# Kernel tuning notes

Hardware: AMD Instinct MI355X
Metric: run time of the kernel (lower is better)

The kernel has to match this reference:

```python
import jax, jax.numpy as jnp
import numpy as np

N_ATOMS = 50000
N_PAIRS = 1600000
N_BASIS = 128
N_FILTERS = 128
N_RBF = 20
LOG2 = float(np.log(2.0))


def ssp(x):
    # ShiftedSoftplus: softplus(x) - log(2)
    return jax.nn.softplus(x) - LOG2


def setup_inputs() -> dict:
    key = jax.random.key(0)
    ks = jax.random.split(key, 16)

    def lin(k, fan_in, fan_out):
        bound = 1.0 / np.sqrt(fan_in)
        kw, kb = jax.random.split(k)
        W = jax.random.uniform(kw, (fan_in, fan_out), jnp.float32, -bound, bound)
        b = jax.random.uniform(kb, (fan_out,), jnp.float32, -bound, bound)
        return W, b

    W_in, b_in = lin(ks[0], N_BASIS, N_FILTERS)
    Wf1, bf1 = lin(ks[1], N_RBF, N_FILTERS)
    Wf2, bf2 = lin(ks[2], N_FILTERS, N_FILTERS)
    Wo1, bo1 = lin(ks[3], N_FILTERS, N_BASIS)
    Wo2, bo2 = lin(ks[4], N_BASIS, N_BASIS)

    return {
        "x": jax.random.normal(ks[5], (N_ATOMS, N_BASIS), jnp.float32),
        "f_ij": jax.random.uniform(ks[6], (N_PAIRS, N_RBF), jnp.float32),
        "rcut_ij": jax.random.uniform(ks[7], (N_PAIRS,), jnp.float32),
        "W_in": W_in, "b_in": b_in,
        "Wf1": Wf1, "bf1": bf1, "Wf2": Wf2, "bf2": bf2,
        "Wo1": Wo1, "bo1": bo1, "Wo2": Wo2, "bo2": bo2,
        "idx_i": jax.random.randint(ks[8], (N_PAIRS,), 0, N_ATOMS, jnp.int32),
        "idx_j": jax.random.randint(ks[9], (N_PAIRS,), 0, N_ATOMS, jnp.int32),
    }


def reference(x, f_ij, rcut_ij, W_in, b_in, Wf1, bf1, Wf2, bf2, Wo1, bo1, Wo2, bo2, idx_i, idx_j):
    # input_to_feature
    h = x @ W_in + b_in                                  # [N, F]
    # filter network: Linear -> ssp -> Linear, then cutoff scaling
    Wij = ssp(f_ij @ Wf1 + bf1) @ Wf2 + bf2              # [E, F]
    Wij = Wij * rcut_ij[:, None]
    # gather - multiply - scatter_add
    x_ij = h[idx_j] * Wij                                # [E, F]
    agg = jax.ops.segment_sum(x_ij, idx_i, num_segments=h.shape[0])  # [N, F]
    # feature_to_output: Linear -> ssp -> Linear
    out = ssp(agg @ Wo1 + bo1) @ Wo2 + bo2               # [N, B]
    return out
```

## Files before the change

kernel.cpp:

```cpp
#include <hip/hip_runtime.h>
#include <math.h>

#define N_ATOMS 50000
#define N_PAIRS 1600000
#define NF 128
#define NRBF 20
#define PADCAP 2050000
#define NTILE_CAP (PADCAP / 16)
#define NBLK 196

typedef _Float16 half8 __attribute__((ext_vector_type(8)));
typedef float floatx4 __attribute__((ext_vector_type(4)));
typedef unsigned long long u64;
typedef u64 u64x2 __attribute__((ext_vector_type(2)));
typedef unsigned short u16;

__device__ __forceinline__ float sspf(float x) {
    float t = __expf(-fabsf(x));
    return fmaxf(x, 0.0f) + __logf(1.0f + t) - 0.69314718055994530942f;
}

__device__ __forceinline__ int permf(int i) { return ((i & 15) << 3) | (i >> 4); }

__device__ __forceinline__ int swz16(int row, int k8) {
    return row * 256 + ((k8 ^ (row & 15)) << 4);
}

__global__ __launch_bounds__(256) void prep_kernel(
    const float* __restrict__ W_in, const float* __restrict__ Wf2,
    const float* __restrict__ Wo1, const float* __restrict__ Wo2,
    _Float16* __restrict__ Wimg, int* __restrict__ woffs)
{
    const int b = blockIdx.x;
    const float* W = (b == 0) ? W_in : (b == 1) ? Wf2 : (b == 2) ? Wo1 : Wo2;
    char* img = (char*)(Wimg + b * 16384);
    for (int i = threadIdx.x; i < 128 * 128; i += 256) {
        int c = i & 127, k = i >> 7;
        float v;
        if (b == 1)      v = W[permf(k) * 128 + permf(c)];
        else if (b == 3) v = W[k * 128 + permf(c)];
        else             v = W[k * 128 + c];
        *(_Float16*)(img + swz16(c, k >> 3) + ((k & 7) << 1)) = (_Float16)v;
    }
    for (int i = b * 256 + threadIdx.x; i < N_ATOMS; i += 1024) woffs[i] = 0;
}

__global__ __launch_bounds__(256) void scanA_kernel(
    const int* __restrict__ cnt, int* __restrict__ bsum)
{
    __shared__ int red[256];
    const int t = threadIdx.x;
    int i = blockIdx.x * 256 + t;
    int c = (i < N_ATOMS) ? cnt[i] : 0;
    red[t] = (c + 15) >> 4;
    __syncthreads();
    for (int s = 128; s > 0; s >>= 1) {
        if (t < s) red[t] += red[t + s];
        __syncthreads();
    }
    if (t == 0) bsum[blockIdx.x] = red[0];
}

__global__ __launch_bounds__(256) void scanB_kernel(
    const int* __restrict__ bsum, int* __restrict__ bpre, int* __restrict__ meta)
{
    __shared__ int sc[256];
    const int t = threadIdx.x;
    int v = (t < NBLK) ? bsum[t] : 0;
    sc[t] = v;
    __syncthreads();
    for (int off = 1; off < 256; off <<= 1) {
        int x = (t >= off) ? sc[t - off] : 0;
        __syncthreads();
        sc[t] += x;
        __syncthreads();
    }
    if (t < NBLK) bpre[t] = sc[t] - v;
    if (t == 255) meta[0] = sc[255] < NTILE_CAP ? sc[255] : NTILE_CAP;
}

__global__ __launch_bounds__(256) void scanC_kernel(
    int* __restrict__ woffs, const int* __restrict__ bpre,
    int* __restrict__ desc)
{
    __shared__ int sc[256];
    const int t = threadIdx.x;
    int i = blockIdx.x * 256 + t;
    int c = (i < N_ATOMS) ? woffs[i] : 0;
    int nt = (c + 15) >> 4;
    sc[t] = nt;
    __syncthreads();
    for (int off = 1; off < 256; off <<= 1) {
        int x = (t >= off) ? sc[t - off] : 0;
        __syncthreads();
        sc[t] += x;
        __syncthreads();
    }
    int tb = bpre[blockIdx.x] + sc[t] - nt;
    if (i < N_ATOMS) {
        woffs[i] = tb * 16;
        for (int k = 0; k < nt; ++k) {
            int nv = c - k * 16; if (nv > 16) nv = 16;
            if (tb + k < NTILE_CAP) desc[tb + k] = (i << 5) | nv;
        }
    }
}

__global__ __launch_bounds__(256) void scatter_kernel(
    const float* __restrict__ f_ij, const float* __restrict__ rcut,
    const int* __restrict__ idx_i, const int* __restrict__ idx_j,
    int* __restrict__ woffs, u64* __restrict__ f_s)
{
    for (int e = blockIdx.x * 256 + threadIdx.x; e < N_PAIRS; e += gridDim.x * 256) {
        int pos = atomicAdd(&woffs[idx_i[e]], 1);
        if (pos >= PADCAP) continue;
        const float4* fr = (const float4*)(f_ij + (size_t)e * NRBF);
        u64 qw[6];
        #pragma unroll
        for (int v = 0; v < 5; ++v) {
            float4 fv = fr[v];
            union { u64 u; _Float16 hx[4]; } pk;
            pk.hx[0] = (_Float16)fv.x; pk.hx[1] = (_Float16)fv.y;
            pk.hx[2] = (_Float16)fv.z; pk.hx[3] = (_Float16)fv.w;
            qw[v] = pk.u;
        }
        qw[5] = (u64)__float_as_uint(rcut[e]) | ((u64)(u16)idx_j[e] << 32);
        u64* dst = f_s + (size_t)pos * 6;
        u64x2 p0 = {qw[0], qw[1]}, p1 = {qw[2], qw[3]}, p2 = {qw[4], qw[5]};
        *(u64x2*)(dst + 0) = p0;
        *(u64x2*)(dst + 2) = p1;
        *(u64x2*)(dst + 4) = p2;
    }
}

template<int NTHR>
__device__ __forceinline__ void stage_img(const _Float16* __restrict__ img, char* dst, int t) {
    const float4* s = (const float4*)img;
    float4* d = (float4*)dst;
    for (int i = t; i < 2048; i += NTHR) d[i] = s[i];
}

template<typename TIN, typename TOUT, bool SSP_OUT, bool ZERO, bool HIST>
__global__ __launch_bounds__(256) void gemm_mfma_kernel(
    const TIN* __restrict__ A, const _Float16* __restrict__ Wimg,
    const float* __restrict__ bias, TOUT* __restrict__ out, int M,
    float* __restrict__ zbuf, int zcount4,
    const int* __restrict__ hidx, int* __restrict__ hcnt)
{
    __shared__ char sW[32768];
    const int t = threadIdx.x;
    const int w = t >> 6, lane = t & 63, m = lane & 15, q = lane >> 4;

    if (ZERO) {
        float4 z = {0.f, 0.f, 0.f, 0.f};
        for (int i = blockIdx.x * 256 + t; i < zcount4; i += gridDim.x * 256)
            ((float4*)zbuf)[i] = z;
    }
    if (HIST) {
        for (int e = blockIdx.x * 256 + t; e < N_PAIRS; e += gridDim.x * 256)
            atomicAdd(&hcnt[hidx[e]], 1);
    }
    stage_img<256>(Wimg, sW, t);
    float bv[8];
    #pragma unroll
    for (int g = 0; g < 8; ++g) bv[g] = bias[g * 16 + m];
    __syncthreads();

    const floatx4 zero4 = {0.f, 0.f, 0.f, 0.f};
    const int ntiles = (M + 63) >> 6;
    for (int tile = blockIdx.x; tile < ntiles; tile += gridDim.x) {
        const int arow = tile * 64 + w * 16 + m;
        half8 a[4];
        if (arow < M) {
            const TIN* ap = A + (size_t)arow * 128;
            #pragma unroll
            for (int s = 0; s < 4; ++s) {
                if (sizeof(TIN) == 2) {
                    a[s] = *(const half8*)(ap + s * 32 + q * 8);
                } else {
                    float4 u0 = *(const float4*)((const float*)ap + s * 32 + q * 8);
                    float4 u1 = *(const float4*)((const float*)ap + s * 32 + q * 8 + 4);
                    a[s][0] = (_Float16)u0.x; a[s][1] = (_Float16)u0.y;
                    a[s][2] = (_Float16)u0.z; a[s][3] = (_Float16)u0.w;
                    a[s][4] = (_Float16)u1.x; a[s][5] = (_Float16)u1.y;
                    a[s][6] = (_Float16)u1.z; a[s][7] = (_Float16)u1.w;
                }
            }
        } else {
            #pragma unroll
            for (int s = 0; s < 4; ++s) a[s] = (half8){};
        }
        floatx4 acc[8];
        #pragma unroll
        for (int g = 0; g < 8; ++g) {
            floatx4 c = zero4;
            #pragma unroll
            for (int s = 0; s < 4; ++s) {
                half8 b = *(const half8*)(sW + swz16(g * 16 + m, 4 * s + q));
                c = __builtin_amdgcn_mfma_f32_16x16x32_f16(a[s], b, c, 0, 0, 0);
            }
            acc[g] = c;
        }
        #pragma unroll
        for (int r = 0; r < 4; ++r) {
            const int grow = tile * 64 + w * 16 + q * 4 + r;
            if (grow < M) {
                TOUT* op = out + (size_t)grow * 128;
                #pragma unroll
                for (int g = 0; g < 8; ++g) {
                    float v = acc[g][r] + bv[g];
                    if (SSP_OUT) v = sspf(v);
                    op[g * 16 + m] = (TOUT)v;
                }
            }
        }
    }
}

__global__ __launch_bounds__(256) void out_kernel(
    const float* __restrict__ A, const _Float16* __restrict__ Wimg1,
    const _Float16* __restrict__ Wimg2, const float* __restrict__ bo1,
    const float* __restrict__ bo2, float* __restrict__ out, int M)
{
    __shared__ char sW[65536];
    __shared__ char sS[4][4096];
    const int t = threadIdx.x;
    const int w = t >> 6, lane = t & 63, m = lane & 15, q = lane >> 4;

    stage_img<256>(Wimg1, sW, t);
    stage_img<256>(Wimg2, sW + 32768, t);
    float b1v[8];
    #pragma unroll
    for (int g = 0; g < 8; ++g) b1v[g] = bo1[g * 16 + m];
    float4 o2lo = *(const float4*)(bo2 + m * 8);
    float4 o2hi = *(const float4*)(bo2 + m * 8 + 4);
    float b2v[8] = {o2lo.x, o2lo.y, o2lo.z, o2lo.w, o2hi.x, o2hi.y, o2hi.z, o2hi.w};
    __syncthreads();

    char* mySS = sS[w];
    const floatx4 zero4 = {0.f, 0.f, 0.f, 0.f};
    const int ntiles = (M + 63) >> 6;
    for (int tile = blockIdx.x; tile < ntiles; tile += gridDim.x) {
        const int arow = tile * 64 + w * 16 + m;
        half8 a[4];
        if (arow < M) {
            const float* ap = A + (size_t)arow * 128;
            #pragma unroll
            for (int s = 0; s < 4; ++s) {
                float4 u0 = *(const float4*)(ap + s * 32 + q * 8);
                float4 u1 = *(const float4*)(ap + s * 32 + q * 8 + 4);
                a[s][0] = (_Float16)u0.x; a[s][1] = (_Float16)u0.y;
                a[s][2] = (_Float16)u0.z; a[s][3] = (_Float16)u0.w;
                a[s][4] = (_Float16)u1.x; a[s][5] = (_Float16)u1.y;
                a[s][6] = (_Float16)u1.z; a[s][7] = (_Float16)u1.w;
            }
        } else {
            #pragma unroll
            for (int s = 0; s < 4; ++s) a[s] = (half8){};
        }
        #pragma unroll
        for (int g = 0; g < 8; ++g) {
            floatx4 c = zero4;
            #pragma unroll
            for (int s = 0; s < 4; ++s) {
                half8 b = *(const half8*)(sW + swz16(g * 16 + m, 4 * s + q));
                c = __builtin_amdgcn_mfma_f32_16x16x32_f16(a[s], b, c, 0, 0, 0);
            }
            #pragma unroll
            for (int r = 0; r < 4; ++r) {
                float v = sspf(c[r] + b1v[g]);
                *(_Float16*)(mySS + swz16(q * 4 + r, 2 * g + (m >> 3)) + ((m & 7) << 1)) =
                    (_Float16)v;
            }
        }
        half8 a2[4];
        #pragma unroll
        for (int s = 0; s < 4; ++s)
            a2[s] = *(const half8*)(mySS + swz16(m, 4 * s + q));
        floatx4 acc[8];
        #pragma unroll
        for (int g = 0; g < 8; ++g) {
            floatx4 c = zero4;
            #pragma unroll
            for (int s = 0; s < 4; ++s) {
                half8 b = *(const half8*)(sW + 32768 + swz16(g * 16 + m, 4 * s + q));
                c = __builtin_amdgcn_mfma_f32_16x16x32_f16(a2[s], b, c, 0, 0, 0);
            }
            acc[g] = c;
        }
        #pragma unroll
        for (int r = 0; r < 4; ++r) {
            const int grow = tile * 64 + w * 16 + q * 4 + r;
            if (grow < M) {
                float* op = out + (size_t)grow * 128 + m * 8;
                float4 lo = {acc[0][r] + b2v[0], acc[1][r] + b2v[1],
                             acc[2][r] + b2v[2], acc[3][r] + b2v[3]};
                float4 hi = {acc[4][r] + b2v[4], acc[5][r] + b2v[5],
                             acc[6][r] + b2v[6], acc[7][r] + b2v[7]};
                *(float4*)op = lo;
                *(float4*)(op + 4) = hi;
            }
        }
    }
}

__global__ __launch_bounds__(256) void edge_kernel(
    const u64* __restrict__ f_s, const int* __restrict__ desc,
    const int* __restrict__ meta,
    const float* __restrict__ Wf1, const float* __restrict__ bf1,
    const _Float16* __restrict__ Wf2img, const float* __restrict__ bf2,
    const _Float16* __restrict__ h, float* __restrict__ agg)
{
    __shared__ char sW2[32768];
    __shared__ char sS[4][4096];
    const int t = threadIdx.x;
    const int w = t >> 6, lane = t & 63, m = lane & 15, q = lane >> 4;

    stage_img<256>(Wf2img, sW2, t);
    half8 bW1[8];
    #pragma unroll
    for (int g = 0; g < 8; ++g) {
        #pragma unroll
        for (int j = 0; j < 8; ++j) {
            int k = q * 8 + j;
            bW1[g][j] = (k < NRBF) ? (_Float16)Wf1[k * 128 + m * 8 + g] : (_Float16)0.0f;
        }
    }
    float4 b1lo = *(const float4*)(bf1 + m * 8), b1hi = *(const float4*)(bf1 + m * 8 + 4);
    float4 b2lo = *(const float4*)(bf2 + m * 8), b2hi = *(const float4*)(bf2 + m * 8 + 4);
    float bf1r[8] = {b1lo.x, b1lo.y, b1lo.z, b1lo.w, b1hi.x, b1hi.y, b1hi.z, b1hi.w};
    float bf2r[8] = {b2lo.x, b2lo.y, b2lo.z, b2lo.w, b2hi.x, b2hi.y, b2hi.z, b2hi.w};
    __syncthreads();

    char* mySS = sS[w];
    const floatx4 zero4 = {0.f, 0.f, 0.f, 0.f};
    const int NT = meta[0];
    const int nw = gridDim.x * 4;
    const int wid = blockIdx.x * 4 + w;
    const int T = (NT + nw - 1) / nw;
    int t0 = wid * T, t1 = t0 + T;
    if (t1 > NT) t1 = NT;
    if (t0 >= t1) return;

    auto loadtile = [&](int tt, int& d_, u64& x0_, u64& x1_, u64* rcj) {
        d_ = desc[tt];
        const u64* base = f_s + (size_t)(tt * 16 + m) * 6;
        u64 x0 = 0, x1 = 0;
        if (q < 2)       { x0 = base[2 * q]; x1 = base[2 * q + 1]; }
        else if (q == 2) { x0 = base[4]; }
        x0_ = x0; x1_ = x1;
        const u64* rbase = f_s + (size_t)(tt * 16 + q * 4) * 6;
        rcj[0] = rbase[5];  rcj[1] = rbase[11];
        rcj[2] = rbase[17]; rcj[3] = rbase[23];
    };

    int d; u64 u0, u1; u64 rcj[4];
    loadtile(t0, d, u0, u1, rcj);

    float racc[8];
    #pragma unroll
    for (int g = 0; g < 8; ++g) racc[g] = 0.f;

    for (int tt = t0; tt < t1; ++tt) {
        const int nv = d & 31;
        const int atom = d >> 5;

        float rc[4]; int jm[4];
        #pragma unroll
        for (int r = 0; r < 4; ++r) {
            bool ok = (q * 4 + r) < nv;
            rc[r] = ok ? __uint_as_float((unsigned)rcj[r]) : 0.f;
            jm[r] = ok ? (int)((rcj[r] >> 32) & 0xffffu) : 0;
        }
        half8 hv[4];
        #pragma unroll
        for (int r = 0; r < 4; ++r)
            hv[r] = *(const half8*)(h + (size_t)jm[r] * NF + m * 8);

        int nd = 0; u64 nu0 = 0, nu1 = 0; u64 nrcj[4] = {0, 0, 0, 0};
        if (tt + 1 < t1) loadtile(tt + 1, nd, nu0, nu1, nrcj);

        union { u64 uu[2]; half8 v; } cv;
        cv.uu[0] = u0; cv.uu[1] = u1;
        half8 a1 = cv.v;
        if (m >= nv) a1 = (half8){};

        floatx4 c1[8];
        #pragma unroll
        for (int g = 0; g < 8; ++g)
            c1[g] = __builtin_amdgcn_mfma_f32_16x16x32_f16(a1, bW1[g], zero4, 0, 0, 0);

        #pragma unroll
        for (int g = 0; g < 8; ++g) {
            #pragma unroll
            for (int r = 0; r < 4; ++r) {
                float v = sspf(c1[g][r] + bf1r[g]);
                *(_Float16*)(mySS + swz16(q * 4 + r, 2 * g + (m >> 3)) + ((m & 7) << 1)) =
                    (_Float16)v;
            }
        }
        half8 a2[4];
        #pragma unroll
        for (int s = 0; s < 4; ++s)
            a2[s] = *(const half8*)(mySS + swz16(m, 4 * s + q));

        #pragma unroll
        for (int g = 0; g < 8; ++g) {
            floatx4 c = zero4;
            #pragma unroll
            for (int s = 0; s < 4; ++s) {
                half8 b = *(const half8*)(sW2 + swz16(g * 16 + m, 4 * s + q));
                c = __builtin_amdgcn_mfma_f32_16x16x32_f16(a2[s], b, c, 0, 0, 0);
            }
            #pragma unroll
            for (int r = 0; r < 4; ++r)
                racc[g] += ((c[r] + bf2r[g]) * rc[r]) * (float)hv[r][g];
        }

        bool last = (tt + 1 >= t1);
        if (last || (nd >> 5) != atom) {
            float* arow = agg + (size_t)atom * NF + m * 8;
            #pragma unroll
            for (int g = 0; g < 8; ++g) {
                float v = racc[g];
                v += __shfl_xor(v, 16, 64);
                v += __shfl_xor(v, 32, 64);
                if (q == 0) atomicAdd(&arow[g], v);
                racc[g] = 0.f;
            }
        }
        d = nd; u0 = nu0; u1 = nu1;
        rcj[0] = nrcj[0]; rcj[1] = nrcj[1]; rcj[2] = nrcj[2]; rcj[3] = nrcj[3];
    }
}

__global__ __launch_bounds__(256) void edge_atomic_kernel(
    const float* __restrict__ f_ij, const float* __restrict__ rcut,
    const float* __restrict__ Wf1, const float* __restrict__ bf1,
    const _Float16* __restrict__ Wf2img, const float* __restrict__ bf2,
    const int* __restrict__ idx_i, const int* __restrict__ idx_j,
    const _Float16* __restrict__ h, float* __restrict__ agg)
{
    __shared__ char sW2[32768];
    __shared__ char sS[4][4096];
    const int NTILES = N_PAIRS / 64;
    const int t = threadIdx.x;
    const int w = t >> 6, lane = t & 63, m = lane & 15, q = lane >> 4;

    stage_img<256>(Wf2img, sW2, t);
    half8 bW1[8];
    #pragma unroll
    for (int g = 0; g < 8; ++g) {
        #pragma unroll
        for (int j = 0; j < 8; ++j) {
            int k = q * 8 + j;
            bW1[g][j] = (k < NRBF) ? (_Float16)Wf1[k * 128 + m * 8 + g] : (_Float16)0.0f;
        }
    }
    float4 b1lo = *(const float4*)(bf1 + m * 8), b1hi = *(const float4*)(bf1 + m * 8 + 4);
    float4 b2lo = *(const float4*)(bf2 + m * 8), b2hi = *(const float4*)(bf2 + m * 8 + 4);
    float bf1r[8] = {b1lo.x, b1lo.y, b1lo.z, b1lo.w, b1hi.x, b1hi.y, b1hi.z, b1hi.w};
    float bf2r[8] = {b2lo.x, b2lo.y, b2lo.z, b2lo.w, b2hi.x, b2hi.y, b2hi.z, b2hi.w};
    __syncthreads();

    char* mySS = sS[w];
    const floatx4 zero4 = {0.f, 0.f, 0.f, 0.f};
    const float4 fz = {0.f, 0.f, 0.f, 0.f};

    for (int tile = blockIdx.x; tile < NTILES; tile += gridDim.x) {
        const int e0 = tile * 64 + w * 16;
        float4 f0 = fz, f1 = fz;
        const float* fb = f_ij + (size_t)(e0 + m) * NRBF + q * 8;
        if (q < 2)      { f0 = *(const float4*)fb; f1 = *(const float4*)(fb + 4); }
        else if (q == 2){ f0 = *(const float4*)fb; }
        int4 jj4 = *(const int4*)&idx_j[e0 + q * 4];
        int4 ii4 = *(const int4*)&idx_i[e0 + q * 4];
        float4 rc4 = *(const float4*)&rcut[e0 + q * 4];
        int jj[4] = {jj4.x, jj4.y, jj4.z, jj4.w};
        half8 hv[4];
        #pragma unroll
        for (int r = 0; r < 4; ++r)
            hv[r] = *(const half8*)(h + (size_t)jj[r] * NF + m * 8);

        half8 a1;
        a1[0]=(_Float16)f0.x; a1[1]=(_Float16)f0.y; a1[2]=(_Float16)f0.z; a1[3]=(_Float16)f0.w;
        a1[4]=(_Float16)f1.x; a1[5]=(_Float16)f1.y; a1[6]=(_Float16)f1.z; a1[7]=(_Float16)f1.w;
        floatx4 c1[8];
        #pragma unroll
        for (int g = 0; g < 8; ++g)
            c1[g] = __builtin_amdgcn_mfma_f32_16x16x32_f16(a1, bW1[g], zero4, 0, 0, 0);

        #pragma unroll
        for (int g = 0; g < 8; ++g) {
            #pragma unroll
            for (int r = 0; r < 4; ++r) {
                float v = sspf(c1[g][r] + bf1r[g]);
                *(_Float16*)(mySS + swz16(q * 4 + r, 2 * g + (m >> 3)) + ((m & 7) << 1)) =
                    (_Float16)v;
            }
        }
        half8 a2[4];
        #pragma unroll
        for (int s = 0; s < 4; ++s)
            a2[s] = *(const half8*)(mySS + swz16(m, 4 * s + q));

        floatx4 acc[8];
        #pragma unroll
        for (int g = 0; g < 8; ++g) {
            floatx4 c = zero4;
            #pragma unroll
            for (int s = 0; s < 4; ++s) {
                half8 b = *(const half8*)(sW2 + swz16(g * 16 + m, 4 * s + q));
                c = __builtin_amdgcn_mfma_f32_16x16x32_f16(a2[s], b, c, 0, 0, 0);
            }
            acc[g] = c;
        }
        int ii[4] = {ii4.x, ii4.y, ii4.z, ii4.w};
        float rc[4] = {rc4.x, rc4.y, rc4.z, rc4.w};
        #pragma unroll
        for (int r = 0; r < 4; ++r) {
            float* arow = agg + (size_t)ii[r] * 128 + m * 8;
            #pragma unroll
            for (int g = 0; g < 8; ++g) {
                float wij = (acc[g][r] + bf2r[g]) * rc[r];
                atomicAdd(&arow[g], (float)hv[r][g] * wij);
            }
        }
    }
}

extern "C" void kernel_launch(void* const* d_in, const int* in_sizes, int n_in,
                              void* d_out, int out_size, void* d_ws, size_t ws_size,
                              hipStream_t stream) {
    const float* x     = (const float*)d_in[0];
    const float* f_ij  = (const float*)d_in[1];
    const float* rcutp = (const float*)d_in[2];
    const float* W_in  = (const float*)d_in[3];
    const float* b_in  = (const float*)d_in[4];
    const float* Wf1   = (const float*)d_in[5];
    const float* bf1   = (const float*)d_in[6];
    const float* Wf2   = (const float*)d_in[7];
    const float* bf2   = (const float*)d_in[8];
    const float* Wo1   = (const float*)d_in[9];
    const float* bo1   = (const float*)d_in[10];
    const float* Wo2   = (const float*)d_in[11];
    const float* bo2   = (const float*)d_in[12];
    const int* idx_i   = (const int*)d_in[13];
    const int* idx_j   = (const int*)d_in[14];
    float* out = (float*)d_out;

    char* ws = (char*)d_ws;
    float*     agg   = (float*)ws;
    _Float16*  h     = (_Float16*)(ws + 25600000);
    _Float16*  Wimg  = (_Float16*)(ws + 38400000);
    int*       woffs = (int*)(ws + 38531072);
    int*       meta  = (int*)(ws + 38731072);
    int*       bsum  = (int*)(ws + 38731088);
    int*       bpre  = (int*)(ws + 38731888);
    int*       desc  = (int*)(ws + 38732688);
    u64*       f_s   = (u64*)(ws + 39245200);
    const size_t NEED = 137645200;

    const int zc4 = N_ATOMS * NF / 4;
    prep_kernel<<<dim3(4), 256, 0, stream>>>(W_in, Wf2, Wo1, Wo2, Wimg, woffs);

    if (ws_size >= NEED) {
        gemm_mfma_kernel<float, _Float16, false, true, true>
            <<<dim3(782), 256, 0, stream>>>(x, Wimg, b_in, h, N_ATOMS, agg, zc4,
                                            idx_i, woffs);
        scanA_kernel<<<dim3(NBLK), 256, 0, stream>>>(woffs, bsum);
        scanB_kernel<<<dim3(1), 256, 0, stream>>>(bsum, bpre, meta);
        scanC_kernel<<<dim3(NBLK), 256, 0, stream>>>(woffs, bpre, desc);
        scatter_kernel<<<dim3(1024), 256, 0, stream>>>(
            f_ij, rcutp, idx_i, idx_j, woffs, f_s);
        edge_kernel<<<dim3(768), 256, 0, stream>>>(
            f_s, desc, meta, Wf1, bf1, Wimg + 16384, bf2, h, agg);
    } else {
        gemm_mfma_kernel<float, _Float16, false, true, false>
            <<<dim3(782), 256, 0, stream>>>(x, Wimg, b_in, h, N_ATOMS, agg, zc4,
                                            nullptr, nullptr);
        edge_atomic_kernel<<<dim3(768), 256, 0, stream>>>(
            f_ij, rcutp, Wf1, bf1, Wimg + 16384, bf2, idx_i, idx_j, h, agg);
    }

    out_kernel<<<dim3(782), 256, 0, stream>>>(
        agg, Wimg + 32768, Wimg + 49152, bo1, bo2, out, N_ATOMS);
}
```

Baseline: 763.4 us.

## Scatter edge IDs instead of packed payloads; convert edge data in GEMM prologue

The scatter kernel now writes only a 4-byte edge id per sorted slot instead of a 48-byte packed payload. The fp16 conversion and packing of f_ij, rcut and idx_j move into the input GEMM prologue and are written in edge order. The edge kernel then reads the payload indirectly through eid_s, trading coalesced reads for gathered ones. Other changes: the edge kernel runs 512 threads per block, the ssp stage writes half8 vectors to LDS with a matching weight permutation, and pad slots are zeroed in scanC.

```diff
diff --git a/kernel.cpp b/kernel.cpp
--- a/kernel.cpp
+++ b/kernel.cpp
@@ -36,10 +36,7 @@
     char* img = (char*)(Wimg + b * 16384);
     for (int i = threadIdx.x; i < 128 * 128; i += 256) {
         int c = i & 127, k = i >> 7;
-        float v;
-        if (b == 1)      v = W[permf(k) * 128 + permf(c)];
-        else if (b == 3) v = W[k * 128 + permf(c)];
-        else             v = W[k * 128 + c];
+        float v = (b == 0) ? W[k * 128 + c] : W[k * 128 + permf(c)];
         *(_Float16*)(img + swz16(c, k >> 3) + ((k & 7) << 1)) = (_Float16)v;
     }
     for (int i = b * 256 + threadIdx.x; i < N_ATOMS; i += 1024) woffs[i] = 0;
@@ -81,7 +78,7 @@
 
 __global__ __launch_bounds__(256) void scanC_kernel(
     int* __restrict__ woffs, const int* __restrict__ bpre,
-    int* __restrict__ desc)
+    int* __restrict__ desc, int* __restrict__ eid_s)
 {
     __shared__ int sc[256];
     const int t = threadIdx.x;
@@ -103,33 +100,18 @@
             int nv = c - k * 16; if (nv > 16) nv = 16;
             if (tb + k < NTILE_CAP) desc[tb + k] = (i << 5) | nv;
         }
-    }
-}
-
-__global__ __launch_bounds__(256) void scatter_kernel(
-    const float* __restrict__ f_ij, const float* __restrict__ rcut,
-    const int* __restrict__ idx_i, const int* __restrict__ idx_j,
-    int* __restrict__ woffs, u64* __restrict__ f_s)
+        int padlo = tb * 16 + c, padhi = (tb + nt) * 16;
+        if (padhi > PADCAP) padhi = PADCAP;
+        for (int s = padlo; s < padhi; ++s) eid_s[s] = 0;
+    }
+}
+
+__global__ __launch_bounds__(256) void scatter_eid_kernel(
+    const int* __restrict__ idx_i, int* __restrict__ woffs, int* __restrict__ eid_s)
 {
     for (int e = blockIdx.x * 256 + threadIdx.x; e < N_PAIRS; e += gridDim.x * 256) {
         int pos = atomicAdd(&woffs[idx_i[e]], 1);
-        if (pos >= PADCAP) continue;
-        const float4* fr = (const float4*)(f_ij + (size_t)e * NRBF);
-        u64 qw[6];
-        #pragma unroll
-        for (int v = 0; v < 5; ++v) {
-            float4 fv = fr[v];
-            union { u64 u; _Float16 hx[4]; } pk;
-            pk.hx[0] = (_Float16)fv.x; pk.hx[1] = (_Float16)fv.y;
-            pk.hx[2] = (_Float16)fv.z; pk.hx[3] = (_Float16)fv.w;
-            qw[v] = pk.u;
-        }
-        qw[5] = (u64)__float_as_uint(rcut[e]) | ((u64)(u16)idx_j[e] << 32);
-        u64* dst = f_s + (size_t)pos * 6;
-        u64x2 p0 = {qw[0], qw[1]}, p1 = {qw[2], qw[3]}, p2 = {qw[4], qw[5]};
-        *(u64x2*)(dst + 0) = p0;
-        *(u64x2*)(dst + 2) = p1;
-        *(u64x2*)(dst + 4) = p2;
+        if (pos < PADCAP) eid_s[pos] = e;
     }
 }
 
@@ -140,12 +122,14 @@
     for (int i = t; i < 2048; i += NTHR) d[i] = s[i];
 }
 
-template<typename TIN, typename TOUT, bool SSP_OUT, bool ZERO, bool HIST>
+template<typename TIN, typename TOUT, bool SSP_OUT, bool ZERO, bool HIST, bool CVT>
 __global__ __launch_bounds__(256) void gemm_mfma_kernel(
     const TIN* __restrict__ A, const _Float16* __restrict__ Wimg,
     const float* __restrict__ bias, TOUT* __restrict__ out, int M,
     float* __restrict__ zbuf, int zcount4,
-    const int* __restrict__ hidx, int* __restrict__ hcnt)
+    const int* __restrict__ hidx, int* __restrict__ hcnt,
+    const float* __restrict__ cf, const float* __restrict__ crc,
+    const int* __restrict__ cj, u64* __restrict__ cdst)
 {
     __shared__ char sW[32768];
     const int t = threadIdx.x;
@@ -159,6 +143,26 @@
     if (HIST) {
         for (int e = blockIdx.x * 256 + t; e < N_PAIRS; e += gridDim.x * 256)
             atomicAdd(&hcnt[hidx[e]], 1);
+    }
+    if (CVT) {
+        for (int e = blockIdx.x * 256 + t; e < N_PAIRS; e += gridDim.x * 256) {
+            const float4* fr = (const float4*)(cf + (size_t)e * NRBF);
+            u64 qw[6];
+            #pragma unroll
+            for (int v = 0; v < 5; ++v) {
+                float4 fv = fr[v];
+                union { u64 u; _Float16 hx[4]; } pk;
+                pk.hx[0] = (_Float16)fv.x; pk.hx[1] = (_Float16)fv.y;
+                pk.hx[2] = (_Float16)fv.z; pk.hx[3] = (_Float16)fv.w;
+                qw[v] = pk.u;
+            }
+            qw[5] = (u64)__float_as_uint(crc[e]) | ((u64)(u16)cj[e] << 32);
+            u64* dst = cdst + (size_t)e * 6;
+            u64x2 p0 = {qw[0], qw[1]}, p1 = {qw[2], qw[3]}, p2 = {qw[4], qw[5]};
+            *(u64x2*)(dst + 0) = p0;
+            *(u64x2*)(dst + 2) = p1;
+            *(u64x2*)(dst + 4) = p2;
+        }
     }
     stage_img<256>(Wimg, sW, t);
     float bv[8];
@@ -229,11 +233,9 @@
 
     stage_img<256>(Wimg1, sW, t);
     stage_img<256>(Wimg2, sW + 32768, t);
-    float b1v[8];
-    #pragma unroll
-    for (int g = 0; g < 8; ++g) b1v[g] = bo1[g * 16 + m];
-    float4 o2lo = *(const float4*)(bo2 + m * 8);
-    float4 o2hi = *(const float4*)(bo2 + m * 8 + 4);
+    float4 o1lo = *(const float4*)(bo1 + m * 8), o1hi = *(const float4*)(bo1 + m * 8 + 4);
+    float4 o2lo = *(const float4*)(bo2 + m * 8), o2hi = *(const float4*)(bo2 + m * 8 + 4);
+    float b1v[8] = {o1lo.x, o1lo.y, o1lo.z, o1lo.w, o1hi.x, o1hi.y, o1hi.z, o1hi.w};
     float b2v[8] = {o2lo.x, o2lo.y, o2lo.z, o2lo.w, o2hi.x, o2hi.y, o2hi.z, o2hi.w};
     __syncthreads();
 
@@ -258,6 +260,7 @@
             #pragma unroll
             for (int s = 0; s < 4; ++s) a[s] = (half8){};
         }
+        floatx4 ct[8];
         #pragma unroll
         for (int g = 0; g < 8; ++g) {
             floatx4 c = zero4;
@@ -266,12 +269,14 @@
                 half8 b = *(const half8*)(sW + swz16(g * 16 + m, 4 * s + q));
                 c = __builtin_amdgcn_mfma_f32_16x16x32_f16(a[s], b, c, 0, 0, 0);
             }
-            #pragma unroll
-            for (int r = 0; r < 4; ++r) {
-                float v = sspf(c[r] + b1v[g]);
-                *(_Float16*)(mySS + swz16(q * 4 + r, 2 * g + (m >> 3)) + ((m & 7) << 1)) =
-                    (_Float16)v;
-            }
+            ct[g] = c;
+        }
+        #pragma unroll
+        for (int r = 0; r < 4; ++r) {
+            half8 hp;
+            #pragma unroll
+            for (int g = 0; g < 8; ++g) hp[g] = (_Float16)sspf(ct[g][r] + b1v[g]);
+            *(half8*)(mySS + swz16(q * 4 + r, m)) = hp;
         }
         half8 a2[4];
         #pragma unroll
@@ -304,19 +309,19 @@
     }
 }
 
-__global__ __launch_bounds__(256) void edge_kernel(
-    const u64* __restrict__ f_s, const int* __restrict__ desc,
-    const int* __restrict__ meta,
+__global__ __launch_bounds__(512) void edge_kernel(
+    const u64* __restrict__ f16c, const int* __restrict__ eid_s,
+    const int* __restrict__ desc, const int* __restrict__ meta,
     const float* __restrict__ Wf1, const float* __restrict__ bf1,
     const _Float16* __restrict__ Wf2img, const float* __restrict__ bf2,
     const _Float16* __restrict__ h, float* __restrict__ agg)
 {
     __shared__ char sW2[32768];
-    __shared__ char sS[4][4096];
+    __shared__ char sS[8][4096];
     const int t = threadIdx.x;
     const int w = t >> 6, lane = t & 63, m = lane & 15, q = lane >> 4;
 
-    stage_img<256>(Wf2img, sW2, t);
+    stage_img<512>(Wf2img, sW2, t);
     half8 bW1[8];
     #pragma unroll
     for (int g = 0; g < 8; ++g) {
@@ -335,8 +340,8 @@
     char* mySS = sS[w];
     const floatx4 zero4 = {0.f, 0.f, 0.f, 0.f};
     const int NT = meta[0];
-    const int nw = gridDim.x * 4;
-    const int wid = blockIdx.x * 4 + w;
+    const int nw = gridDim.x * 8;
+    const int wid = blockIdx.x * 8 + w;
     const int T = (NT + nw - 1) / nw;
     int t0 = wid * T, t1 = t0 + T;
     if (t1 > NT) t1 = NT;
@@ -344,14 +349,17 @@
 
     auto loadtile = [&](int tt, int& d_, u64& x0_, u64& x1_, u64* rcj) {
         d_ = desc[tt];
-        const u64* base = f_s + (size_t)(tt * 16 + m) * 6;
+        int4 e4 = *(const int4*)&eid_s[tt * 16 + q * 4];
+        int em = eid_s[tt * 16 + m];
+        const u64* base = f16c + (size_t)em * 6;
         u64 x0 = 0, x1 = 0;
         if (q < 2)       { x0 = base[2 * q]; x1 = base[2 * q + 1]; }
         else if (q == 2) { x0 = base[4]; }
         x0_ = x0; x1_ = x1;
-        const u64* rbase = f_s + (size_t)(tt * 16 + q * 4) * 6;
-        rcj[0] = rbase[5];  rcj[1] = rbase[11];
-        rcj[2] = rbase[17]; rcj[3] = rbase[23];
+        rcj[0] = f16c[(size_t)e4.x * 6 + 5];
+        rcj[1] = f16c[(size_t)e4.y * 6 + 5];
+        rcj[2] = f16c[(size_t)e4.z * 6 + 5];
+        rcj[3] = f16c[(size_t)e4.w * 6 + 5];
     };
 
     int d; u64 u0, u1; u64 rcj[4];
@@ -391,13 +399,11 @@
             c1[g] = __builtin_amdgcn_mfma_f32_16x16x32_f16(a1, bW1[g], zero4, 0, 0, 0);
 
         #pragma unroll
-        for (int g = 0; g < 8; ++g) {
-            #pragma unroll
-            for (int r = 0; r < 4; ++r) {
-                float v = sspf(c1[g][r] + bf1r[g]);
-                *(_Float16*)(mySS + swz16(q * 4 + r, 2 * g + (m >> 3)) + ((m & 7) << 1)) =
-                    (_Float16)v;
-            }
+        for (int r = 0; r < 4; ++r) {
+            half8 hp;
+            #pragma unroll
+            for (int g = 0; g < 8; ++g) hp[g] = (_Float16)sspf(c1[g][r] + bf1r[g]);
+            *(half8*)(mySS + swz16(q * 4 + r, m)) = hp;
         }
         half8 a2[4];
         #pragma unroll
@@ -491,13 +497,11 @@
             c1[g] = __builtin_amdgcn_mfma_f32_16x16x32_f16(a1, bW1[g], zero4, 0, 0, 0);
 
         #pragma unroll
-        for (int g = 0; g < 8; ++g) {
-            #pragma unroll
-            for (int r = 0; r < 4; ++r) {
-                float v = sspf(c1[g][r] + bf1r[g]);
-                *(_Float16*)(mySS + swz16(q * 4 + r, 2 * g + (m >> 3)) + ((m & 7) << 1)) =
-                    (_Float16)v;
-            }
+        for (int r = 0; r < 4; ++r) {
+            half8 hp;
+            #pragma unroll
+            for (int g = 0; g < 8; ++g) hp[g] = (_Float16)sspf(c1[g][r] + bf1r[g]);
+            *(half8*)(mySS + swz16(q * 4 + r, m)) = hp;
         }
         half8 a2[4];
         #pragma unroll
@@ -558,26 +562,27 @@
     int*       bsum  = (int*)(ws + 38731088);
     int*       bpre  = (int*)(ws + 38731888);
     int*       desc  = (int*)(ws + 38732688);
-    u64*       f_s   = (u64*)(ws + 39245200);
-    const size_t NEED = 137645200;
+    int*       eid_s = (int*)(ws + 39245200);
+    u64*       f16c  = (u64*)(ws + 47445200);
+    const size_t NEED = 124245200;
 
     const int zc4 = N_ATOMS * NF / 4;
     prep_kernel<<<dim3(4), 256, 0, stream>>>(W_in, Wf2, Wo1, Wo2, Wimg, woffs);
 
     if (ws_size >= NEED) {
-        gemm_mfma_kernel<float, _Float16, false, true, true>
+        gemm_mfma_kernel<float, _Float16, false, true, true, true>
             <<<dim3(782), 256, 0, stream>>>(x, Wimg, b_in, h, N_ATOMS, agg, zc4,
-                                            idx_i, woffs);
+                                            idx_i, woffs, f_ij, rcutp, idx_j, f16c);
         scanA_kernel<<<dim3(NBLK), 256, 0, stream>>>(woffs, bsum);
         scanB_kernel<<<dim3(1), 256, 0, stream>>>(bsum, bpre, meta);
-        scanC_kernel<<<dim3(NBLK), 256, 0, stream>>>(woffs, bpre, desc);
-        scatter_kernel<<<dim3(1024), 256, 0, stream>>>(
-            f_ij, rcutp, idx_i, idx_j, woffs, f_s);
-        edge_kernel<<<dim3(768), 256, 0, stream>>>(
-            f_s, desc, meta, Wf1, bf1, Wimg + 16384, bf2, h, agg);
+        scanC_kernel<<<dim3(NBLK), 256, 0, stream>>>(woffs, bpre, desc, eid_s);
+        scatter_eid_kernel<<<dim3(1024), 256, 0, stream>>>(idx_i, woffs, eid_s);
+        edge_kernel<<<dim3(512), 512, 0, stream>>>(
+            f16c, eid_s, desc, meta, Wf1, bf1, Wimg + 16384, bf2, h, agg);
     } else {
-        gemm_mfma_kernel<float, _Float16, false, true, false>
+        gemm_mfma_kernel<float, _Float16, false, true, false, false>
             <<<dim3(782), 256, 0, stream>>>(x, Wimg, b_in, h, N_ATOMS, agg, zc4,
+                                            nullptr, nullptr, nullptr, nullptr,
                                             nullptr, nullptr);
         edge_atomic_kernel<<<dim3(768), 256, 0, stream>>>(
             f_ij, rcutp, Wf1, bf1, Wimg + 16384, bf2, idx_i, idx_j, h, agg);
```

Result: slower. 900.8 us (+18.0%).

## Vectorize ssp scratch stores via permuted weight layout and enlarge edge blocks

Applied to the files above, without the earlier changes.

The hidden-activation scratch writes in the edge and output kernels now pack eight fp16 values into one half8 LDS store per row, replacing scalar 2-byte stores. To make this work, the weight images for Wf2 and Wo1/Wo2 are prepared with a column-only permutation so the packed layout matches the MFMA fragment order, and bias vectors are loaded contiguously. The edge kernel also moves from 768 blocks of 256 threads to 512 blocks of 768 threads (12 waves), sharing one staged Wf2 image across more waves. This cuts LDS store instructions and staging traffic per wave, but risks register pressure from holding all eight accumulators live and lower occupancy under launch_bounds(768).

```diff
diff --git a/kernel.cpp b/kernel.cpp
--- a/kernel.cpp
+++ b/kernel.cpp
@@ -36,10 +36,7 @@
     char* img = (char*)(Wimg + b * 16384);
     for (int i = threadIdx.x; i < 128 * 128; i += 256) {
         int c = i & 127, k = i >> 7;
-        float v;
-        if (b == 1)      v = W[permf(k) * 128 + permf(c)];
-        else if (b == 3) v = W[k * 128 + permf(c)];
-        else             v = W[k * 128 + c];
+        float v = (b == 0) ? W[k * 128 + c] : W[k * 128 + permf(c)];
         *(_Float16*)(img + swz16(c, k >> 3) + ((k & 7) << 1)) = (_Float16)v;
     }
     for (int i = b * 256 + threadIdx.x; i < N_ATOMS; i += 1024) woffs[i] = 0;
@@ -229,11 +226,9 @@
 
     stage_img<256>(Wimg1, sW, t);
     stage_img<256>(Wimg2, sW + 32768, t);
-    float b1v[8];
-    #pragma unroll
-    for (int g = 0; g < 8; ++g) b1v[g] = bo1[g * 16 + m];
-    float4 o2lo = *(const float4*)(bo2 + m * 8);
-    float4 o2hi = *(const float4*)(bo2 + m * 8 + 4);
+    float4 o1lo = *(const float4*)(bo1 + m * 8), o1hi = *(const float4*)(bo1 + m * 8 + 4);
+    float4 o2lo = *(const float4*)(bo2 + m * 8), o2hi = *(const float4*)(bo2 + m * 8 + 4);
+    float b1v[8] = {o1lo.x, o1lo.y, o1lo.z, o1lo.w, o1hi.x, o1hi.y, o1hi.z, o1hi.w};
     float b2v[8] = {o2lo.x, o2lo.y, o2lo.z, o2lo.w, o2hi.x, o2hi.y, o2hi.z, o2hi.w};
     __syncthreads();
 
@@ -258,6 +253,7 @@
             #pragma unroll
             for (int s = 0; s < 4; ++s) a[s] = (half8){};
         }
+        floatx4 ct[8];
         #pragma unroll
         for (int g = 0; g < 8; ++g) {
             floatx4 c = zero4;
@@ -266,12 +262,14 @@
                 half8 b = *(const half8*)(sW + swz16(g * 16 + m, 4 * s + q));
                 c = __builtin_amdgcn_mfma_f32_16x16x32_f16(a[s], b, c, 0, 0, 0);
             }
-            #pragma unroll
-            for (int r = 0; r < 4; ++r) {
-                float v = sspf(c[r] + b1v[g]);
-                *(_Float16*)(mySS + swz16(q * 4 + r, 2 * g + (m >> 3)) + ((m & 7) << 1)) =
-                    (_Float16)v;
-            }
+            ct[g] = c;
+        }
+        #pragma unroll
+        for (int r = 0; r < 4; ++r) {
+            half8 hp;
+            #pragma unroll
+            for (int g = 0; g < 8; ++g) hp[g] = (_Float16)sspf(ct[g][r] + b1v[g]);
+            *(half8*)(mySS + swz16(q * 4 + r, m)) = hp;
         }
         half8 a2[4];
         #pragma unroll
@@ -304,7 +302,7 @@
     }
 }
 
-__global__ __launch_bounds__(256) void edge_kernel(
+__global__ __launch_bounds__(768) void edge_kernel(
     const u64* __restrict__ f_s, const int* __restrict__ desc,
     const int* __restrict__ meta,
     const float* __restrict__ Wf1, const float* __restrict__ bf1,
@@ -312,11 +310,11 @@
     const _Float16* __restrict__ h, float* __restrict__ agg)
 {
     __shared__ char sW2[32768];
-    __shared__ char sS[4][4096];
+    __shared__ char sS[12][4096];
     const int t = threadIdx.x;
     const int w = t >> 6, lane = t & 63, m = lane & 15, q = lane >> 4;
 
-    stage_img<256>(Wf2img, sW2, t);
+    stage_img<768>(Wf2img, sW2, t);
     half8 bW1[8];
     #pragma unroll
     for (int g = 0; g < 8; ++g) {
@@ -335,8 +333,8 @@
     char* mySS = sS[w];
     const floatx4 zero4 = {0.f, 0.f, 0.f, 0.f};
     const int NT = meta[0];
-    const int nw = gridDim.x * 4;
-    const int wid = blockIdx.x * 4 + w;
+    const int nw = gridDim.x * 12;
+    const int wid = blockIdx.x * 12 + w;
     const int T = (NT + nw - 1) / nw;
     int t0 = wid * T, t1 = t0 + T;
     if (t1 > NT) t1 = NT;
@@ -349,9 +347,9 @@
         if (q < 2)       { x0 = base[2 * q]; x1 = base[2 * q + 1]; }
         else if (q == 2) { x0 = base[4]; }
         x0_ = x0; x1_ = x1;
-        const u64* rbase = f_s + (size_t)(tt * 16 + q * 4) * 6;
-        rcj[0] = rbase[5];  rcj[1] = rbase[11];
-        rcj[2] = rbase[17]; rcj[3] = rbase[23];
+        const u64* rb = f_s + (size_t)(tt * 16 + q * 4) * 6 + 5;
+        rcj[0] = rb[0];  rcj[1] = rb[6];
+        rcj[2] = rb[12]; rcj[3] = rb[18];
     };
 
     int d; u64 u0, u1; u64 rcj[4];
@@ -391,13 +389,11 @@
             c1[g] = __builtin_amdgcn_mfma_f32_16x16x32_f16(a1, bW1[g], zero4, 0, 0, 0);
 
         #pragma unroll
-        for (int g = 0; g < 8; ++g) {
-            #pragma unroll
-            for (int r = 0; r < 4; ++r) {
-                float v = sspf(c1[g][r] + bf1r[g]);
-                *(_Float16*)(mySS + swz16(q * 4 + r, 2 * g + (m >> 3)) + ((m & 7) << 1)) =
-                    (_Float16)v;
-            }
+        for (int r = 0; r < 4; ++r) {
+            half8 hp;
+            #pragma unroll
+            for (int g = 0; g < 8; ++g) hp[g] = (_Float16)sspf(c1[g][r] + bf1r[g]);
+            *(half8*)(mySS + swz16(q * 4 + r, m)) = hp;
         }
         half8 a2[4];
         #pragma unroll
@@ -491,13 +487,11 @@
             c1[g] = __builtin_amdgcn_mfma_f32_16x16x32_f16(a1, bW1[g], zero4, 0, 0, 0);
 
         #pragma unroll
-        for (int g = 0; g < 8; ++g) {
-            #pragma unroll
-            for (int r = 0; r < 4; ++r) {
-                float v = sspf(c1[g][r] + bf1r[g]);
-                *(_Float16*)(mySS + swz16(q * 4 + r, 2 * g + (m >> 3)) + ((m & 7) << 1)) =
-                    (_Float16)v;
-            }
+        for (int r = 0; r < 4; ++r) {
+            half8 hp;
+            #pragma unroll
+            for (int g = 0; g < 8; ++g) hp[g] = (_Float16)sspf(c1[g][r] + bf1r[g]);
+            *(half8*)(mySS + swz16(q * 4 + r, m)) = hp;
         }
         half8 a2[4];
         #pragma unroll
@@ -573,7 +567,7 @@
         scanC_kernel<<<dim3(NBLK), 256, 0, stream>>>(woffs, bpre, desc);
         scatter_kernel<<<dim3(1024), 256, 0, stream>>>(
             f_ij, rcutp, idx_i, idx_j, woffs, f_s);
-        edge_kernel<<<dim3(768), 256, 0, stream>>>(
+        edge_kernel<<<dim3(512), 768, 0, stream>>>(
             f_s, desc, meta, Wf1, bf1, Wimg + 16384, bf2, h, agg);
     } else {
         gemm_mfma_kernel<float, _Float16, false, true, false>
```

New measurement: 1.150 ms. 50.6% more time.
